# Kernel tuning notes

Measured on AMD Instinct MI355X. Metric: run time of the kernel, lower is better.

Reference implementation:

```python
import jax, jax.numpy as jnp
import numpy as np

B, N_ENC, N_DEC = 32, 512, 512
IN_V, OUT_V = 2000, 2000
H, F, K, P = 256, 256, 5, 4  # P = |G| (indices < P are masked to 0 before embedding)
E_ENC, E_DEC = 128, 128


def setup_inputs() -> dict:
    key = jax.random.key(0)
    ks = jax.random.split(key, 16)
    s = lambda i, shape, scale=0.05: jax.random.normal(ks[i], shape, jnp.float32) * scale
    return dict(
        xs_idx=jax.random.randint(ks[0], (B, N_ENC), 0, IN_V),
        ys_idx=jax.random.randint(ks[1], (B, N_DEC), 0, OUT_V),
        gembed_W=s(2, (IN_V, F)),
        gconv_W=s(3, (K, F, F)),
        gdecode_W=s(4, (F, OUT_V)),
        enc_embed=s(5, (IN_V, E_ENC)),
        dec_embed=s(6, (OUT_V, E_DEC)),
        enc_Wih=s(7, (4 * H, E_ENC)),
        enc_Whh=s(8, (4 * H, H)),
        enc_b=jnp.zeros((4 * H,), jnp.float32),
        dec_Wih=s(9, (4 * H, E_DEC)),
        dec_Whh=s(10, (4 * H, H)),
        dec_b=jnp.zeros((4 * H,), jnp.float32),
        T=jax.random.uniform(ks[11], (H, 2 * H), jnp.float32, -0.5, 0.5),
    )


def _lstm(x, Wih, Whh, b, h0, c0):
    # x: (B, T, D); PyTorch gate order i, f, g, o
    def step(carry, xt):
        h, c = carry
        z = xt @ Wih.T + h @ Whh.T + b
        i, f, g, o = jnp.split(z, 4, axis=-1)
        c = jax.nn.sigmoid(f) * c + jax.nn.sigmoid(i) * jnp.tanh(g)
        h = jax.nn.sigmoid(o) * jnp.tanh(c)
        return (h, c), h
    (hT, cT), hs = jax.lax.scan(step, (h0, c0), jnp.swapaxes(x, 0, 1))
    return jnp.swapaxes(hs, 0, 1), hT, cT


def reference(xs_idx, ys_idx, gembed_W, gconv_W, gdecode_W, enc_embed, dec_embed,
              enc_Wih, enc_Whh, enc_b, dec_Wih, dec_Whh, dec_b, T):
    # --- G-equivariant stack: per-encoder-position distribution over output vocab ---
    e = jnp.tanh(gembed_W[xs_idx])  # (B, Ne, F)
    c = jax.lax.conv_general_dilated(e, gconv_W, (1,), 'SAME',
                                     dimension_numbers=('NWC', 'WIO', 'NWC'))
    probs = jax.nn.softmax(jnp.tanh(c) @ gdecode_W, axis=-1)  # (B, Ne, V)
    # encoder_scores[b, i, j] = probs[b, i, ys[b, j]]
    idx = jnp.broadcast_to(ys_idx[:, None, :], (probs.shape[0], probs.shape[1], ys_idx.shape[1]))
    encoder_scores = jnp.take_along_axis(probs, idx, axis=2)  # (B, Ne, Nd)

    # --- invariant LSTM encoder (indices < |G| masked to 0) ---
    xm = jnp.where(xs_idx < P, 0, xs_idx)
    x_embed = enc_embed[xm]  # (B, Ne, E)
    z = jnp.zeros((x_embed.shape[0], H), jnp.float32)
    henc, hT, cT = _lstm(x_embed, enc_Wih, enc_Whh, enc_b, z, z)
    hback, _, _ = _lstm(jnp.flip(x_embed, axis=1), enc_Wih, enc_Whh, enc_b, z, z)
    hback = jnp.flip(hback, axis=1)

    # --- decoder LSTM, initialized with encoder final state ---
    ym = jnp.where(ys_idx < P, 0, ys_idx)
    y_embed = dec_embed[ym]
    out, _, _ = _lstm(y_embed, dec_Wih, dec_Whh, dec_b, hT, cT)
    h_dec = jnp.concatenate([henc[:, -1:, :], out], axis=1)[:, :-1, :]  # (B, Nd, H)
    h_enc = jnp.concatenate([henc, hback], axis=2)  # (B, Ne, 2H)

    # --- bilinear alignment scores: eij[b, i, j] = h_dec[b, j] . (T @ h_enc[b, i]) ---
    Th = jnp.einsum('he,bie->bih', T, h_enc)           # (B, Ne, H)
    eij = jnp.einsum('bjh,bih->bij', h_dec, Th)        # (B, Ne, Nd)
    align = jax.nn.softmax(eij, axis=1)                # softmax over encoder positions

    p = jnp.sum(jnp.log(jnp.sum(encoder_scores * align, axis=1)), axis=1)  # (B,)
    return -jnp.sum(p)
```

## Files before the change

kernel.cpp:

```cpp
#include <hip/hip_runtime.h>

typedef _Float16 f16;
typedef _Float16 f16x2 __attribute__((ext_vector_type(2)));
typedef _Float16 f16x4 __attribute__((ext_vector_type(4)));
typedef _Float16 f16x8 __attribute__((ext_vector_type(8)));
typedef float    f32x4 __attribute__((ext_vector_type(4)));
typedef int      i32x4 __attribute__((ext_vector_type(4)));
typedef unsigned int u32;
typedef unsigned short u16;

#define DEVI static __device__ __forceinline__

static constexpr int LDT = 40;
static constexpr int LDA = 264;

DEVI float sigf(float x){ return 1.f/(1.f + __expf(-x)); }
DEVI float tanh_c(float x){
  x = fminf(fmaxf(x, -15.f), 15.f);
  float e = __expf(2.f*x);
  return (e - 1.f)/(e + 1.f);
}
DEVI float sig_f(float x){ return __builtin_amdgcn_rcpf(1.f + __expf(-x)); }
DEVI float tanh_f(float x){ return 1.f - 2.f*__builtin_amdgcn_rcpf(1.f + __expf(2.f*x)); }
DEVI float wmax16(float v){
  #pragma unroll
  for (int m=1;m<16;m<<=1) v = fmaxf(v, __shfl_xor(v, m, 64));
  return v;
}
DEVI float wsum16(float v){
  #pragma unroll
  for (int m=1;m<16;m<<=1) v += __shfl_xor(v, m, 64);
  return v;
}
DEVI f16x8 frag_ld(const f16* p){ return *(const f16x8*)p; }
DEVI void stage_tileh(int t256, const f16* src, int ld, f16* dst){
  int row = t256>>2, qq = t256&3;
  *(f16x8*)(dst + row*LDT + qq*8) = *(const f16x8*)(src + (size_t)row*ld + qq*8);
}
#define ZERO4(acc) { f32x4 _z = {0.f,0.f,0.f,0.f}; acc[0]=_z; acc[1]=_z; acc[2]=_z; acc[3]=_z; }

DEVI void gemm64h(int t256, const f16* A, int lda, const f16* Bm, int ldb, int K,
                  f16* lA, f16* lB, f32x4 acc[4]){
  const int lane = t256 & 63, wv = t256 >> 6;
  const int l15 = lane & 15, kq = lane >> 4;
  for (int k0=0; k0<K; k0+=32){
    __syncthreads();
    stage_tileh(t256, A + k0, lda, lA);
    stage_tileh(t256, Bm + k0, ldb, lB);
    __syncthreads();
    f16x8 af = frag_ld(lA + (16*wv + l15)*LDT + kq*8);
    #pragma unroll
    for (int nt=0; nt<4; nt++){
      f16x8 bf = frag_ld(lB + (16*nt + l15)*LDT + kq*8);
      acc[nt] = __builtin_amdgcn_mfma_f32_16x16x32_f16(af, bf, acc[nt], 0,0,0);
    }
  }
}

__global__ void k_cvt(const float* __restrict__ s, f16* __restrict__ d, int n){
  int i = blockIdx.x*256 + threadIdx.x;
  if (i < n) d[i] = (f16)s[i];
}
__global__ void k_gconvT(const float* __restrict__ s, f16* __restrict__ d){
  int id = blockIdx.x;
  int fo = threadIdx.x;
  d[(size_t)fo*1280 + id] = (f16)s[(size_t)id*256 + fo];
}
__global__ void k_gdecT(const float* __restrict__ s, f16* __restrict__ d){
  int v = blockIdx.x, f = threadIdx.x;
  f16 val = (f16)0.f;
  if (v < 2000) val = (f16)s[(size_t)f*2000 + v];
  d[(size_t)v*256 + f] = val;
}
__global__ void k_epad(const int* __restrict__ xs, const float* __restrict__ gemb, f16* __restrict__ epad){
  int id = blockIdx.x;
  int f = threadIdx.x;
  int b = id / 516, p = id % 516;
  float v = 0.f;
  if (p >= 2 && p < 514){ int idx = xs[b*512 + p - 2]; v = tanh_c(gemb[(size_t)idx*256 + f]); }
  epad[(size_t)id*256 + f] = (f16)v;
}
__global__ void k_embx(const int* __restrict__ xs, const int* __restrict__ ys,
                       const float* __restrict__ eemb, const float* __restrict__ demb,
                       f16* __restrict__ xo, f16* __restrict__ yo){
  int id = blockIdx.x; int f = threadIdx.x;
  bool dec = id >= 32*512; int id2 = dec ? id - 32*512 : id;
  int idx = dec ? ys[id2] : xs[id2];
  if (idx < 4) idx = 0;
  const float* src = (dec ? demb : eemb) + (size_t)idx*128;
  (dec ? yo : xo)[(size_t)id2*128 + f] = (f16)src[f];
}

__global__ void k_wmax(const float* __restrict__ Whh, u32* __restrict__ ws){
  int i = (blockIdx.x*256 + threadIdx.x)*4;
  float m = 0.f;
  #pragma unroll
  for (int j=0;j<4;j++) m = fmaxf(m, fabsf(Whh[i+j]));
  #pragma unroll
  for (int d=1; d<64; d<<=1) m = fmaxf(m, __shfl_xor(m, d, 64));
  if ((threadIdx.x & 63) == 0) atomicMax(ws, __float_as_uint(m));
}
__global__ void k_wq8(const float* __restrict__ Whh, const u32* __restrict__ ws,
                      i32x4* __restrict__ Wq){
  const int bid = blockIdx.x;
  const int l = threadIdx.x;
  const int kt = bid & 3, t8 = (bid >> 2) & 7, w = bid >> 5;
  const int r15 = l & 15;
  const int u4 = r15 >> 2, g = r15 & 3;
  const int unit = w*32 + t8*4 + u4;
  const int row = g*256 + unit;
  const int k0  = kt*64 + (l >> 4)*16;
  const float scale = 127.f / __uint_as_float(ws[0]);
  int dw[4];
  #pragma unroll
  for (int d=0; d<4; d++){
    u32 acc = 0;
    #pragma unroll
    for (int j=0; j<4; j++){
      float q = __builtin_rintf(Whh[(size_t)row*256 + k0 + d*4 + j] * scale);
      int qi = (int)fminf(fmaxf(q, -127.f), 127.f);
      acc |= ((u32)qi & 0xffu) << (8*j);
    }
    dw[d] = (int)acc;
  }
  i32x4 v = { dw[0], dw[1], dw[2], dw[3] };
  Wq[(size_t)bid*64 + l] = v;
}

__global__ __launch_bounds__(256,4) void k_conv(const f16* __restrict__ epad, const f16* __restrict__ gcT, f16* __restrict__ tf){
  __shared__ f16 lA[64*LDT], lB[64*LDT];
  const int m0 = blockIdx.x*64, n0 = blockIdx.y*64;
  const int b = m0 >> 9, n = m0 & 511;
  f32x4 acc[4]; ZERO4(acc);
  gemm64h(threadIdx.x, epad + ((size_t)b*516 + n)*256, 256, gcT + (size_t)n0*1280, 1280, 1280, lA, lB, acc);
  const int lane=threadIdx.x&63, wv=threadIdx.x>>6, l15=lane&15, kq=lane>>4;
  #pragma unroll
  for (int nt=0;nt<4;nt++)
    #pragma unroll
    for (int r=0;r<4;r++)
      tf[(size_t)(m0 + 16*wv + 4*kq + r)*256 + n0 + nt*16 + l15] = (f16)tanh_c(acc[nt][r]);
}

DEVI void ku_body(int t256, int m0, int n0, const f16* X, const f16* Wih,
                  const float* bias, f16* U, f16* lA, f16* lB){
  f32x4 acc[4]; ZERO4(acc);
  gemm64h(t256, X + (size_t)m0*128, 128, Wih + (size_t)n0*128, 128, 128, lA, lB, acc);
  const int lane=t256&63, wv=t256>>6, l15=lane&15, kq=lane>>4;
  #pragma unroll
  for (int nt=0;nt<4;nt++){
    int n = n0 + nt*16 + l15;
    float bv = bias[n];
    int cnew = (n & 255)*4 + (n >> 8);
    #pragma unroll
    for (int r=0;r<4;r++)
      U[(size_t)(m0 + 16*wv + 4*kq + r)*1024 + cnew] = (f16)(acc[nt][r] + bv);
  }
}

__global__ __launch_bounds__(256,4) void k_u(const f16* __restrict__ X, const f16* __restrict__ Wih,
                                             const float* __restrict__ bias, f16* __restrict__ U){
  __shared__ f16 lA[64*LDT], lB[64*LDT];
  ku_body(threadIdx.x, blockIdx.x*64, blockIdx.y*64, X, Wih, bias, U, lA, lB);
}

DEVI void th_body(int t256, int m0, int n0, const f16* henh, const f16* Tf, f16* Th,
                  f16* lA, f16* lB){
  f32x4 acc[4]; ZERO4(acc);
  gemm64h(t256, henh + (size_t)m0*512, 512, Tf + (size_t)n0*512, 512, 512, lA, lB, acc);
  const int lane=t256&63, wv=t256>>6, l15=lane&15, kq=lane>>4;
  #pragma unroll
  for (int nt=0;nt<4;nt++)
    #pragma unroll
    for (int r=0;r<4;r++)
      Th[(size_t)(m0 + 16*wv + 4*kq + r)*256 + n0 + nt*16 + l15] = (f16)acc[nt][r];
}

DEVI void pass1_body(int tid, int mt, int ns, const f16* tf, const f16* gdT,
                     float* mxp, float* sep, f16* lA, f16* lB2, float* mxs2, float* ses2){
  const int half = tid >> 8, t256 = tid & 255;
  const int lane = tid & 63, wv = t256 >> 6, l15 = lane & 15, kq = lane >> 4;
  f16* lB = lB2 + half*(64*LDT);
  {
    const f16* A = tf + (size_t)mt*64*256;
    int row = tid >> 3, c8 = tid & 7;
    #pragma unroll
    for (int q=0;q<4;q++)
      *(f16x8*)(lA + row*LDA + c8*32 + q*8) = *(const f16x8*)(A + (size_t)row*256 + c8*32 + q*8);
  }
  if (t256 < 64){ mxs2[half*64 + t256] = -1e30f; ses2[half*64 + t256] = 0.f; }
  __syncthreads();
  for (int nci=0; nci<4; nci++){
    const int nc = half*4 + nci;
    const int nbase = ns*512 + nc*64;
    const f16* Bm = gdT + (size_t)nbase*256;
    f32x4 acc[4]; ZERO4(acc);
    for (int k0=0; k0<256; k0+=32){
      __syncthreads();
      stage_tileh(t256, Bm + k0, 256, lB);
      __syncthreads();
      f16x8 af = frag_ld(lA + (16*wv + l15)*LDA + k0 + kq*8);
      #pragma unroll
      for (int nt=0; nt<4; nt++){
        f16x8 bf = frag_ld(lB + (16*nt + l15)*LDT + kq*8);
        acc[nt] = __builtin_amdgcn_mfma_f32_16x16x32_f16(af, bf, acc[nt], 0,0,0);
      }
    }
    #pragma unroll
    for (int r=0;r<4;r++){
      float av[4]; float cm = -1e30f;
      #pragma unroll
      for (int nt=0;nt<4;nt++){
        int gcol = nbase + nt*16 + l15;
        float a = (gcol < 2000) ? acc[nt][r] : -1e30f;
        av[nt] = a; cm = fmaxf(cm, a);
      }
      cm = wmax16(cm);
      int rr = half*64 + 16*wv + 4*kq + r;
      float old = mxs2[rr];
      float nm = fmaxf(old, cm);
      float ss = 0.f;
      #pragma unroll
      for (int nt=0;nt<4;nt++) ss += __expf(av[nt] - nm);
      ss = wsum16(ss);
      if (l15 == 0){
        ses2[rr] = ses2[rr]*__expf(old - nm) + ss;
        mxs2[rr] = nm;
      }
    }
  }
  __syncthreads();
  if (tid < 64){
    float m0 = mxs2[tid], m1 = mxs2[64+tid];
    float nm = fmaxf(m0, m1);
    float se = ses2[tid]*__expf(m0-nm) + ses2[64+tid]*__expf(m1-nm);
    mxp[(size_t)ns*16384 + mt*64 + tid] = nm;
    sep[(size_t)ns*16384 + mt*64 + tid] = se;
  }
}

__global__ void k_comb1(const float* __restrict__ mxp, const float* __restrict__ sep,
                        float* __restrict__ mx, float* __restrict__ se){
  int m = blockIdx.x*256 + threadIdx.x;
  float best = -1e30f;
  #pragma unroll
  for (int k=0;k<4;k++) best = fmaxf(best, mxp[(size_t)k*16384 + m]);
  float s = 0.f;
  #pragma unroll
  for (int k=0;k<4;k++) s += sep[(size_t)k*16384 + m] * __expf(mxp[(size_t)k*16384 + m] - best);
  mx[m] = best; se[m] = s;
}

DEVI void pass2_body(int t256, int it, int jt, int b, const f16* tf, const f16* gdT,
                     const int* ys, const float* mx, const float* se, f16* scT,
                     f16* lA, f16* lB, int* jv){
  const int lane=t256&63, wv=t256>>6, l15=lane&15, kq=lane>>4;
  if (t256<64) jv[t256] = ys[b*512 + jt*64 + t256];
  const f16* A = tf + ((size_t)b*512 + it*64)*256;
  f32x4 acc[4]; ZERO4(acc);
  for (int k0=0;k0<256;k0+=32){
    __syncthreads();
    stage_tileh(t256, A + k0, 256, lA);
    { int row=t256>>2, qq=t256&3;
      *(f16x8*)(lB + row*LDT + qq*8) = *(const f16x8*)(gdT + (size_t)jv[row]*256 + k0 + qq*8); }
    __syncthreads();
    f16x8 af = frag_ld(lA + (16*wv+l15)*LDT + kq*8);
    #pragma unroll
    for (int nt=0;nt<4;nt++){
      f16x8 bf = frag_ld(lB + (16*nt+l15)*LDT + kq*8);
      acc[nt] = __builtin_amdgcn_mfma_f32_16x16x32_f16(af, bf, acc[nt], 0,0,0);
    }
  }
  float mxv[4], rsev[4];
  #pragma unroll
  for (int r=0;r<4;r++){
    int i_ = it*64 + 16*wv + 4*kq + r;
    mxv[r] = mx[b*512 + i_];
    rsev[r] = 1.f / se[b*512 + i_];
  }
  #pragma unroll
  for (int nt=0;nt<4;nt++){
    int j_ = jt*64 + nt*16 + l15;
    #pragma unroll
    for (int r=0;r<4;r++){
      int i_ = it*64 + 16*wv + 4*kq + r;
      scT[((size_t)b*512 + j_)*512 + i_] = (f16)(__expf(acc[nt][r] - mxv[r]) * rsev[r]);
    }
  }
}

__global__ __launch_bounds__(256,2) void k_final(const f16* __restrict__ hdec, const f16* __restrict__ Th,
                                                 const f16* __restrict__ scT,
                                                 float* __restrict__ pmx, float* __restrict__ pden, float* __restrict__ pnum){
  __shared__ f16 lA[64*LDA];
  __shared__ f16 lB[64*LDT];
  __shared__ float mx_s[64], den_s[64], num_s[64];
  const int is = blockIdx.x, jt = blockIdx.y, b = blockIdx.z;
  const int tid = threadIdx.x, lane=tid&63, wv=tid>>6, l15=lane&15, kq=lane>>4;
  {
    const f16* A = hdec + ((size_t)b*512 + jt*64)*256;
    int row = tid>>2, qq = tid&3;
    #pragma unroll
    for (int c=0;c<8;c++)
      *(f16x8*)(lA + row*LDA + c*32 + qq*8) = *(const f16x8*)(A + (size_t)row*256 + c*32 + qq*8);
  }
  if (tid<64){ mx_s[tid]=-1e30f; den_s[tid]=0.f; num_s[tid]=0.f; }
  __syncthreads();
  for (int ic=0; ic<4; ic++){
    const int i0 = is*256 + ic*64;
    const f16* Bm = Th + ((size_t)b*512 + i0)*256;
    f32x4 acc[4]; ZERO4(acc);
    for (int k0=0;k0<256;k0+=32){
      __syncthreads();
      stage_tileh(tid, Bm + k0, 256, lB);
      __syncthreads();
      f16x8 af = frag_ld(lA + (16*wv+l15)*LDA + k0 + kq*8);
      #pragma unroll
      for (int nt=0;nt<4;nt++){
        f16x8 bf = frag_ld(lB + (16*nt+l15)*LDT + kq*8);
        acc[nt] = __builtin_amdgcn_mfma_f32_16x16x32_f16(af, bf, acc[nt], 0,0,0);
      }
    }
    #pragma unroll
    for (int r=0;r<4;r++){
      int jl = 16*wv + 4*kq + r;
      float av[4]; float cm=-1e30f;
      #pragma unroll
      for (int nt=0;nt<4;nt++){ av[nt]=acc[nt][r]; cm=fmaxf(cm,av[nt]); }
      cm = wmax16(cm);
      float old = mx_s[jl], nm = fmaxf(old, cm);
      float ds=0.f, nsum=0.f;
      const size_t srow = ((size_t)b*512 + jt*64 + jl)*512;
      #pragma unroll
      for (int nt=0;nt<4;nt++){
        float e = __expf(av[nt]-nm);
        float sc = (float)scT[srow + i0 + nt*16 + l15];
        ds += e; nsum += sc*e;
      }
      ds = wsum16(ds); nsum = wsum16(nsum);
      if (l15==0){
        float fac = __expf(old-nm);
        den_s[jl] = den_s[jl]*fac + ds;
        num_s[jl] = num_s[jl]*fac + nsum;
        mx_s[jl] = nm;
      }
    }
  }
  __syncthreads();
  if (tid<64){
    size_t idx = (((size_t)b*512) + jt*64 + tid)*2 + is;
    pmx[idx]=mx_s[tid]; pden[idx]=den_s[tid]; pnum[idx]=num_s[tid];
  }
}

__global__ void k_comb2(const float* __restrict__ pmx, const float* __restrict__ pden,
                        const float* __restrict__ pnum, float* __restrict__ out){
  const int b = blockIdx.x, j = threadIdx.x;
  size_t base = ((size_t)b*512 + j)*2;
  float m0=pmx[base], m1=pmx[base+1];
  float m = fmaxf(m0,m1);
  float e0=__expf(m0-m), e1=__expf(m1-m);
  float den = pden[base]*e0 + pden[base+1]*e1;
  float num = pnum[base]*e0 + pnum[base+1]*e1;
  float lp = __logf(num) - __logf(den);
  __shared__ float red[512];
  red[j] = lp;
  __syncthreads();
  for (int st=256; st>0; st>>=1){ if (j<st) red[j]+=red[j+st]; __syncthreads(); }
  if (j==0) atomicAdd(out, -red[0]);
}

DEVI void lstm_core(char* smem, const f16* U, const i32x4* Wq, const u32* ws,
                    u16* hout, float* hTcT, u16* hdec0, int nsteps, int mode, int bid)
{
  char* h8b = smem;
  const int tid = threadIdx.x;
  const int lane = tid & 63, w = tid >> 6;
  const int l15 = lane & 15, kq = lane >> 4;
  const int s = l15 & 3, p = l15 >> 2;
  const int uA = w*32 + 8*p + kq;
  const int uB = uA + 4;

  int dir = 0, b0;
  if (mode == 0){ dir = bid >> 3; b0 = (bid & 7)*4; }
  else b0 = bid*4;

  const float zscale = __uint_as_float(ws[0]) * (1.f/(127.f*127.f));

  i32x4 aw[32];
  #pragma unroll
  for (int f=0; f<32; f++) aw[f] = Wq[(size_t)(w*32 + f)*64 + lane];

  float cA = 0.f, cB = 0.f;
  if (mode == 0){
    ((u32*)h8b)[tid] = 0u;
  } else {
    const float* hp = hTcT + (size_t)(b0+s)*512;
    float hA = hp[uA], hB = hp[uB];
    cA = hp[256 + uA]; cB = hp[256 + uB];
    h8b[((uA>>4)*4 + s)*16 + (uA&15)] = (char)(int)__builtin_rintf(hA*127.f);
    h8b[((uB>>4)*4 + s)*16 + (uB&15)] = (char)(int)__builtin_rintf(hB*127.f);
  }

  const f16* Urow = U + (size_t)(b0+s)*512*1024;
  f16x4 uvA, uvB;
  {
    int tp0 = dir ? (nsteps-1) : 0;
    uvA = *(const f16x4*)(Urow + (size_t)tp0*1024 + uA*4);
    uvB = *(const f16x4*)(Urow + (size_t)tp0*1024 + uB*4);
  }
  __syncthreads();

  int cur = 0;
  #pragma unroll 1
  for (int t=0; t<nsteps; ++t){
    const int tpos = dir ? (nsteps-1-t) : t;
    int tn = dir ? (nsteps-2-t >= 0 ? nsteps-2-t : 0) : (t+1 < nsteps ? t+1 : nsteps-1);
    f16x4 puA = *(const f16x4*)(Urow + (size_t)tn*1024 + uA*4);
    f16x4 puB = *(const f16x4*)(Urow + (size_t)tn*1024 + uB*4);

    const char* hc = h8b + cur*1024;
    i32x4 bf[4];
    #pragma unroll
    for (int kt=0; kt<4; kt++)
      bf[kt] = *(const i32x4*)(hc + ((kt*4 + kq)*4 + s)*16);

    i32x4 acc[8];
    #pragma unroll
    for (int t8=0; t8<8; t8++){
      i32x4 d = {0,0,0,0};
      #pragma unroll
      for (int kt=0; kt<4; kt++)
        d = __builtin_amdgcn_mfma_i32_16x16x64_i8(aw[t8*4+kt], bf[kt], d, 0,0,0);
      acc[t8] = d;
    }

    i32x4 vA, vB;
    #pragma unroll
    for (int e=0; e<4; e++){
      int x0 = (p&1) ? acc[2][e] : acc[0][e];
      int x1 = (p&1) ? acc[6][e] : acc[4][e];
      vA[e] = (p&2) ? x1 : x0;
      int y0 = (p&1) ? acc[3][e] : acc[1][e];
      int y1 = (p&1) ? acc[7][e] : acc[5][e];
      vB[e] = (p&2) ? y1 : y0;
    }

    float hA_, hB_;
    {
      float z0 = fmaf((float)vA[0], zscale, (float)uvA[0]);
      float z1 = fmaf((float)vA[1], zscale, (float)uvA[1]);
      float z2 = fmaf((float)vA[2], zscale, (float)uvA[2]);
      float z3 = fmaf((float)vA[3], zscale, (float)uvA[3]);
      cA = sig_f(z1)*cA + sig_f(z0)*tanh_f(z2);
      hA_ = sig_f(z3)*tanh_f(cA);
    }
    {
      float z0 = fmaf((float)vB[0], zscale, (float)uvB[0]);
      float z1 = fmaf((float)vB[1], zscale, (float)uvB[1]);
      float z2 = fmaf((float)vB[2], zscale, (float)uvB[2]);
      float z3 = fmaf((float)vB[3], zscale, (float)uvB[3]);
      cB = sig_f(z1)*cB + sig_f(z0)*tanh_f(z2);
      hB_ = sig_f(z3)*tanh_f(cB);
    }

    const int nxt = cur ^ 1;
    char* hn = h8b + nxt*1024;
    hn[((uA>>4)*4 + s)*16 + (uA&15)] = (char)(int)__builtin_rintf(hA_*127.f);
    hn[((uB>>4)*4 + s)*16 + (uB&15)] = (char)(int)__builtin_rintf(hB_*127.f);

    f16 fA = (f16)hA_, fB = (f16)hB_;
    if (mode == 0){
      u16* hr = hout + ((size_t)(b0+s)*512 + tpos)*512 + dir*256;
      hr[uA] = __builtin_bit_cast(u16, fA);
      hr[uB] = __builtin_bit_cast(u16, fB);
      if (!dir && t == nsteps-1){
        hdec0[(size_t)(b0+s)*512*256 + uA] = __builtin_bit_cast(u16, fA);
        hdec0[(size_t)(b0+s)*512*256 + uB] = __builtin_bit_cast(u16, fB);
        float* hp = hTcT + (size_t)(b0+s)*512;
        hp[uA] = hA_; hp[uB] = hB_;
        hp[256+uA] = cA; hp[256+uB] = cB;
      }
    } else {
      u16* hr = hout + ((size_t)(b0+s)*512 + (t+1))*256;
      hr[uA] = __builtin_bit_cast(u16, fA);
      hr[uB] = __builtin_bit_cast(u16, fB);
    }

    asm volatile("s_waitcnt lgkmcnt(0)" ::: "memory");
    __builtin_amdgcn_s_barrier();
    asm volatile("" ::: "memory");
    __builtin_amdgcn_sched_barrier(0);

    cur = nxt;
    uvA = puA; uvB = puB;
  }
}

__global__ __launch_bounds__(512,2) void k_mega_enc(
    const f16* __restrict__ Uenc, const i32x4* __restrict__ Wqe, const u32* __restrict__ wse,
    u16* __restrict__ henh, float* __restrict__ hTcT, u16* __restrict__ hdec0,
    const f16* __restrict__ tf, const f16* __restrict__ gdT,
    float* __restrict__ mxp, float* __restrict__ sep,
    const f16* __restrict__ yemb, const f16* __restrict__ Wihd,
    const float* __restrict__ db, f16* __restrict__ Udec)
{
  __shared__ __align__(16) char smem[45056];
  const int bid = blockIdx.x;
  const int tid = threadIdx.x;
  if (bid < 16){
    lstm_core(smem, Uenc, Wqe, wse, henh, hTcT, hdec0, 512, 0, bid);
    return;
  }
  if (bid >= 256 && bid < 272) return;
  const int w = (bid < 256) ? (bid - 16) : (bid - 32);
  for (int v = w; v < 3072; v += 480){
    __syncthreads();
    if (v < 1024){
      int mt = v >> 2;
      int ns = v & 3;
      pass1_body(tid, mt, ns, tf, gdT, mxp, sep,
                 (f16*)smem, (f16*)(smem + 33792), (float*)(smem + 44032), (float*)(smem + 44544));
    } else {
      int vb = v - 1024;
      int half = tid >> 8, t256 = tid & 255;
      int vbm = vb >> 4, ny = vb & 15;
      int m0 = (vbm*2 + half)*64;
      int n0 = ny*64;
      char* base = smem + half*10240;
      ku_body(t256, m0, n0, yemb, Wihd, db, Udec, (f16*)base, (f16*)(base + 5120));
    }
  }
}

__global__ __launch_bounds__(512,2) void k_mega_dec(
    const f16* __restrict__ Udec, const i32x4* __restrict__ Wqd, const u32* __restrict__ wsd,
    u16* __restrict__ hdec, float* __restrict__ hTcT,
    const f16* __restrict__ tf, const f16* __restrict__ gdT, const int* __restrict__ ys,
    const float* __restrict__ mx, const float* __restrict__ se, f16* __restrict__ scT,
    const f16* __restrict__ henh, const f16* __restrict__ Tf, f16* __restrict__ Th)
{
  __shared__ __align__(16) char smem[24576];
  const int bid = blockIdx.x;
  const int tid = threadIdx.x;
  if (bid < 8){
    lstm_core(smem, Udec, Wqd, wsd, hdec, hTcT, hdec, 511, 1, bid);
    return;
  }
  if (bid >= 256 && bid < 264) return;
  const int w = (bid < 256) ? (bid - 8) : (bid - 16);
  for (int v = w; v < 1536; v += 496){
    __syncthreads();
    if (v < 1024){
      int half = tid >> 8, t256 = tid & 255;
      int b = v >> 5, rem = v & 31;
      int jt = rem >> 2, it = (rem & 3)*2 + half;
      char* base = smem + half*10496;
      pass2_body(t256, it, jt, b, tf, gdT, ys, mx, se, scT,
                 (f16*)base, (f16*)(base + 5120), (int*)(base + 10240));
    } else {
      int vb = v - 1024;
      int half = tid >> 8, t256 = tid & 255;
      int m0 = ((vb >> 2)*2 + half)*64;
      int n0 = (vb & 3)*64;
      char* base = smem + half*10240;
      th_body(t256, m0, n0, henh, Tf, Th, (f16*)base, (f16*)(base + 5120));
    }
  }
}

extern "C" void kernel_launch(void* const* d_in, const int* in_sizes, int n_in,
                              void* d_out, int out_size, void* d_ws, size_t ws_size,
                              hipStream_t stream)
{
  (void)in_sizes; (void)n_in; (void)out_size;
  const int*   xs    = (const int*)d_in[0];
  const int*   ys    = (const int*)d_in[1];
  const float* gemb  = (const float*)d_in[2];
  const float* gconv = (const float*)d_in[3];
  const float* gdec  = (const float*)d_in[4];
  const float* eemb  = (const float*)d_in[5];
  const float* demb  = (const float*)d_in[6];
  const float* eWih  = (const float*)d_in[7];
  const float* eWhh  = (const float*)d_in[8];
  const float* eb    = (const float*)d_in[9];
  const float* dWih  = (const float*)d_in[10];
  const float* dWhh  = (const float*)d_in[11];
  const float* db    = (const float*)d_in[12];
  const float* Tm    = (const float*)d_in[13];

  char* wsb = (char*)d_ws;
  size_t off = 0;
  auto take = [&](size_t bytes)->char*{ char* p = wsb + off; off += (bytes + 255) & ~(size_t)255; return p; };
  f16* epad  = (f16*)take((size_t)32*516*256*2);
  f16* tf    = (f16*)take((size_t)32*512*256*2);
  f16* xemb  = (f16*)take((size_t)32*512*128*2);
  f16* yemb  = (f16*)take((size_t)32*512*128*2);
  f16* Uenc  = (f16*)take((size_t)32*512*1024*2);
  f16* Udec  = (f16*)take((size_t)32*512*1024*2);
  f16* henh  = (f16*)take((size_t)32*512*512*2);
  f16* hdec  = (f16*)take((size_t)32*512*256*2);
  f16* Th    = (f16*)take((size_t)32*512*256*2);
  f16* scT   = (f16*)take((size_t)32*512*512*2);
  float* mx  = (float*)take((size_t)16384*4);
  float* se  = (float*)take((size_t)16384*4);
  float* mxp = (float*)take((size_t)4*16384*4);
  float* sep = (float*)take((size_t)4*16384*4);
  float* pmx = (float*)take((size_t)32*512*2*4);
  float* pden= (float*)take((size_t)32*512*2*4);
  float* pnum= (float*)take((size_t)32*512*2*4);
  float* hTcT= (float*)take((size_t)32*512*4);
  f16* Wihe  = (f16*)take((size_t)1024*128*2);
  f16* Wihd  = (f16*)take((size_t)1024*128*2);
  f16* Tf    = (f16*)take((size_t)256*512*2);
  f16* gcT   = (f16*)take((size_t)256*1280*2);
  f16* gdT   = (f16*)take((size_t)2048*256*2);
  i32x4* Wq8e = (i32x4*)take((size_t)256*64*16);
  i32x4* Wq8d = (i32x4*)take((size_t)256*64*16);
  u32* wsc   = (u32*)take(8);
  if (off > ws_size) return;

  hipMemsetAsync(d_out, 0, sizeof(float), stream);
  hipMemsetAsync(wsc, 0, 8, stream);

  k_cvt<<<dim3(512),  256, 0, stream>>>(eWih, Wihe, 1024*128);
  k_cvt<<<dim3(512),  256, 0, stream>>>(dWih, Wihd, 1024*128);
  k_cvt<<<dim3(512),  256, 0, stream>>>(Tm,   Tf,   256*512);
  k_gconvT<<<dim3(1280), 256, 0, stream>>>(gconv, gcT);
  k_gdecT <<<dim3(2048), 256, 0, stream>>>(gdec, gdT);
  k_wmax<<<dim3(256), 256, 0, stream>>>(eWhh, wsc + 0);
  k_wmax<<<dim3(256), 256, 0, stream>>>(dWhh, wsc + 1);
  k_wq8<<<dim3(256), 64, 0, stream>>>(eWhh, wsc + 0, Wq8e);
  k_wq8<<<dim3(256), 64, 0, stream>>>(dWhh, wsc + 1, Wq8d);
  k_epad<<<dim3(32*516), 256, 0, stream>>>(xs, gemb, epad);
  k_embx<<<dim3(2*32*512), 128, 0, stream>>>(xs, ys, eemb, demb, xemb, yemb);

  k_conv<<<dim3(256,4), 256, 0, stream>>>(epad, gcT, tf);
  k_u<<<dim3(256,16), 256, 0, stream>>>(xemb, Wihe, eb, Uenc);

  k_mega_enc<<<dim3(512), 512, 0, stream>>>(Uenc, Wq8e, wsc + 0, (u16*)henh, hTcT, (u16*)hdec,
                                            tf, gdT, mxp, sep, yemb, Wihd, db, Udec);
  k_comb1<<<dim3(64), 256, 0, stream>>>(mxp, sep, mx, se);

  k_mega_dec<<<dim3(512), 512, 0, stream>>>(Udec, Wq8d, wsc + 1, (u16*)hdec, hTcT,
                                            tf, gdT, ys, mx, se, scT, henh, Tf, Th);

  k_final<<<dim3(2,8,32), 256, 0, stream>>>(hdec, Th, scT, pmx, pden, pnum);
  k_comb2<<<dim3(32), 512, 0, stream>>>(pmx, pden, pnum, (float*)d_out);
}
```

Baseline: 1.134 ms.

## Split LSTM recurrence across twice as many blocks with two batch rows each

Each LSTM block now handles 2 batch rows instead of 4, so each lane computes one hidden unit rather than two, and the number of recurrence blocks doubles (32 encoder, 16 decoder). The point is to shorten the per-step serial work on the critical recurrent path: less gate math per lane and a smaller shared h buffer. In exchange, fewer blocks are left for the overlapped side work (the vocab softmax and projection passes). The MFMA B operand is also half-filled, so matrix throughput per block drops.

After: 981.0 us. 1.16x faster.

```diff
diff --git a/kernel.cpp b/kernel.cpp
--- a/kernel.cpp
+++ b/kernel.cpp
@@ -14,7 +14,6 @@
 static constexpr int LDT = 40;
 static constexpr int LDA = 264;
 
-DEVI float sigf(float x){ return 1.f/(1.f + __expf(-x)); }
 DEVI float tanh_c(float x){
   x = fminf(fmaxf(x, -15.f), 15.f);
   float e = __expf(2.f*x);
@@ -376,13 +375,13 @@
   const int tid = threadIdx.x;
   const int lane = tid & 63, w = tid >> 6;
   const int l15 = lane & 15, kq = lane >> 4;
-  const int s = l15 & 3, p = l15 >> 2;
-  const int uA = w*32 + 8*p + kq;
-  const int uB = uA + 4;
+  const int s = l15 & 1;
+  const int r = l15 >> 1;
+  const int u = w*32 + r*4 + kq;
 
   int dir = 0, b0;
-  if (mode == 0){ dir = bid >> 3; b0 = (bid & 7)*4; }
-  else b0 = bid*4;
+  if (mode == 0){ dir = bid >> 4; b0 = (bid & 15)*2; }
+  else b0 = bid*2;
 
   const float zscale = __uint_as_float(ws[0]) * (1.f/(127.f*127.f));
 
@@ -390,23 +389,21 @@
   #pragma unroll
   for (int f=0; f<32; f++) aw[f] = Wq[(size_t)(w*32 + f)*64 + lane];
 
-  float cA = 0.f, cB = 0.f;
+  float c = 0.f;
   if (mode == 0){
-    ((u32*)h8b)[tid] = 0u;
+    if (tid < 256) ((u32*)h8b)[tid] = 0u;
   } else {
     const float* hp = hTcT + (size_t)(b0+s)*512;
-    float hA = hp[uA], hB = hp[uB];
-    cA = hp[256 + uA]; cB = hp[256 + uB];
-    h8b[((uA>>4)*4 + s)*16 + (uA&15)] = (char)(int)__builtin_rintf(hA*127.f);
-    h8b[((uB>>4)*4 + s)*16 + (uB&15)] = (char)(int)__builtin_rintf(hB*127.f);
+    float h0 = hp[u];
+    c = hp[256 + u];
+    h8b[((u>>4)*2 + s)*16 + (u&15)] = (char)(int)__builtin_rintf(h0*127.f);
   }
 
   const f16* Urow = U + (size_t)(b0+s)*512*1024;
-  f16x4 uvA, uvB;
+  f16x4 uv;
   {
     int tp0 = dir ? (nsteps-1) : 0;
-    uvA = *(const f16x4*)(Urow + (size_t)tp0*1024 + uA*4);
-    uvB = *(const f16x4*)(Urow + (size_t)tp0*1024 + uB*4);
+    uv = *(const f16x4*)(Urow + (size_t)tp0*1024 + u*4);
   }
   __syncthreads();
 
@@ -415,14 +412,13 @@
   for (int t=0; t<nsteps; ++t){
     const int tpos = dir ? (nsteps-1-t) : t;
     int tn = dir ? (nsteps-2-t >= 0 ? nsteps-2-t : 0) : (t+1 < nsteps ? t+1 : nsteps-1);
-    f16x4 puA = *(const f16x4*)(Urow + (size_t)tn*1024 + uA*4);
-    f16x4 puB = *(const f16x4*)(Urow + (size_t)tn*1024 + uB*4);
-
-    const char* hc = h8b + cur*1024;
+    f16x4 pu = *(const f16x4*)(Urow + (size_t)tn*1024 + u*4);
+
+    const char* hc = h8b + cur*512;
     i32x4 bf[4];
     #pragma unroll
     for (int kt=0; kt<4; kt++)
-      bf[kt] = *(const i32x4*)(hc + ((kt*4 + kq)*4 + s)*16);
+      bf[kt] = *(const i32x4*)(hc + ((kt*4 + kq)*2 + s)*16);
 
     i32x4 acc[8];
     #pragma unroll
@@ -434,56 +430,42 @@
       acc[t8] = d;
     }
 
-    i32x4 vA, vB;
+    i32x4 v;
     #pragma unroll
     for (int e=0; e<4; e++){
-      int x0 = (p&1) ? acc[2][e] : acc[0][e];
-      int x1 = (p&1) ? acc[6][e] : acc[4][e];
-      vA[e] = (p&2) ? x1 : x0;
-      int y0 = (p&1) ? acc[3][e] : acc[1][e];
-      int y1 = (p&1) ? acc[7][e] : acc[5][e];
-      vB[e] = (p&2) ? y1 : y0;
-    }
-
-    float hA_, hB_;
+      int x01 = (r&1) ? acc[1][e] : acc[0][e];
+      int x23 = (r&1) ? acc[3][e] : acc[2][e];
+      int x45 = (r&1) ? acc[5][e] : acc[4][e];
+      int x67 = (r&1) ? acc[7][e] : acc[6][e];
+      int y0  = (r&2) ? x23 : x01;
+      int y1  = (r&2) ? x67 : x45;
+      v[e] = (r&4) ? y1 : y0;
+    }
+
+    float h_;
     {
-      float z0 = fmaf((float)vA[0], zscale, (float)uvA[0]);
-      float z1 = fmaf((float)vA[1], zscale, (float)uvA[1]);
-      float z2 = fmaf((float)vA[2], zscale, (float)uvA[2]);
-      float z3 = fmaf((float)vA[3], zscale, (float)uvA[3]);
-      cA = sig_f(z1)*cA + sig_f(z0)*tanh_f(z2);
-      hA_ = sig_f(z3)*tanh_f(cA);
-    }
-    {
-      float z0 = fmaf((float)vB[0], zscale, (float)uvB[0]);
-      float z1 = fmaf((float)vB[1], zscale, (float)uvB[1]);
-      float z2 = fmaf((float)vB[2], zscale, (float)uvB[2]);
-      float z3 = fmaf((float)vB[3], zscale, (float)uvB[3]);
-      cB = sig_f(z1)*cB + sig_f(z0)*tanh_f(z2);
-      hB_ = sig_f(z3)*tanh_f(cB);
+      float z0 = fmaf((float)v[0], zscale, (float)uv[0]);
+      float z1 = fmaf((float)v[1], zscale, (float)uv[1]);
+      float z2 = fmaf((float)v[2], zscale, (float)uv[2]);
+      float z3 = fmaf((float)v[3], zscale, (float)uv[3]);
+      c  = sig_f(z1)*c + sig_f(z0)*tanh_f(z2);
+      h_ = sig_f(z3)*tanh_f(c);
     }
 
     const int nxt = cur ^ 1;
-    char* hn = h8b + nxt*1024;
-    hn[((uA>>4)*4 + s)*16 + (uA&15)] = (char)(int)__builtin_rintf(hA_*127.f);
-    hn[((uB>>4)*4 + s)*16 + (uB&15)] = (char)(int)__builtin_rintf(hB_*127.f);
-
-    f16 fA = (f16)hA_, fB = (f16)hB_;
+    char* hn = h8b + nxt*512;
+    hn[((u>>4)*2 + s)*16 + (u&15)] = (char)(int)__builtin_rintf(h_*127.f);
+
+    f16 fh = (f16)h_;
     if (mode == 0){
-      u16* hr = hout + ((size_t)(b0+s)*512 + tpos)*512 + dir*256;
-      hr[uA] = __builtin_bit_cast(u16, fA);
-      hr[uB] = __builtin_bit_cast(u16, fB);
+      hout[(((size_t)(b0+s)*512 + tpos)*512) + dir*256 + u] = __builtin_bit_cast(u16, fh);
       if (!dir && t == nsteps-1){
-        hdec0[(size_t)(b0+s)*512*256 + uA] = __builtin_bit_cast(u16, fA);
-        hdec0[(size_t)(b0+s)*512*256 + uB] = __builtin_bit_cast(u16, fB);
+        hdec0[(size_t)(b0+s)*512*256 + u] = __builtin_bit_cast(u16, fh);
         float* hp = hTcT + (size_t)(b0+s)*512;
-        hp[uA] = hA_; hp[uB] = hB_;
-        hp[256+uA] = cA; hp[256+uB] = cB;
+        hp[u] = h_; hp[256+u] = c;
       }
     } else {
-      u16* hr = hout + ((size_t)(b0+s)*512 + (t+1))*256;
-      hr[uA] = __builtin_bit_cast(u16, fA);
-      hr[uB] = __builtin_bit_cast(u16, fB);
+      hout[((size_t)(b0+s)*512 + (t+1))*256 + u] = __builtin_bit_cast(u16, fh);
     }
 
     asm volatile("s_waitcnt lgkmcnt(0)" ::: "memory");
@@ -492,7 +474,7 @@
     __builtin_amdgcn_sched_barrier(0);
 
     cur = nxt;
-    uvA = puA; uvB = puB;
+    uv = pu;
   }
 }
 
@@ -507,13 +489,13 @@
   __shared__ __align__(16) char smem[45056];
   const int bid = blockIdx.x;
   const int tid = threadIdx.x;
-  if (bid < 16){
+  if (bid < 32){
     lstm_core(smem, Uenc, Wqe, wse, henh, hTcT, hdec0, 512, 0, bid);
     return;
   }
-  if (bid >= 256 && bid < 272) return;
-  const int w = (bid < 256) ? (bid - 16) : (bid - 32);
-  for (int v = w; v < 3072; v += 480){
+  if (bid >= 256 && bid < 288) return;
+  const int w = (bid < 256) ? (bid - 32) : (bid - 64);
+  for (int v = w; v < 3072; v += 448){
     __syncthreads();
     if (v < 1024){
       int mt = v >> 2;
@@ -542,13 +524,13 @@
   __shared__ __align__(16) char smem[24576];
   const int bid = blockIdx.x;
   const int tid = threadIdx.x;
-  if (bid < 8){
+  if (bid < 16){
     lstm_core(smem, Udec, Wqd, wsd, hdec, hTcT, hdec, 511, 1, bid);
     return;
   }
-  if (bid >= 256 && bid < 264) return;
-  const int w = (bid < 256) ? (bid - 8) : (bid - 16);
-  for (int v = w; v < 1536; v += 496){
+  if (bid >= 256 && bid < 272) return;
+  const int w = (bid < 256) ? (bid - 16) : (bid - 32);
+  for (int v = w; v < 1536; v += 480){
     __syncthreads();
     if (v < 1024){
       int half = tid >> 8, t256 = tid & 255;
```
